# Kernel tuning notes

Measured on AMD Instinct MI355X. Metric: run time of the kernel, lower is better.

## Reference

```python
import jax, jax.numpy as jnp
import numpy as np
import math

D_MODEL = 1024
LAYER_ID = 6
NUM_LAYERS = 12
B, T = 8, 2048
MIN_P = -1e38


def _init_params():
    C = D_MODEL
    r01 = LAYER_ID / (NUM_LAYERS - 1)
    r1a0 = 1.0 - LAYER_ID / NUM_LAYERS
    h = np.arange(C, dtype=np.float32)
    decay_speed = -5.0 + 8.0 * (h / (C - 1)) ** (0.7 + 1.3 * r01)
    zigzag = (((np.arange(C) + 1) % 3) - 1).astype(np.float32) * 0.5
    U = np.float32(math.log(0.3)) + zigzag
    xx = (np.arange(C, dtype=np.float32) / C).reshape(1, 1, C)
    tmk = xx ** r1a0
    tmv = xx ** r1a0 + 0.3 * r01
    tmr = xx ** (0.5 * r1a0)
    return (jnp.asarray(decay_speed), jnp.asarray(U), jnp.asarray(tmk, jnp.float32),
            jnp.asarray(tmv, jnp.float32), jnp.asarray(tmr, jnp.float32))


def setup_inputs() -> dict:
    key = jax.random.key(0)
    k0, k1, k2, k3, k4 = jax.random.split(key, 5)
    W, U, tmk, tmv, tmr = _init_params()
    C = D_MODEL
    s = 1.0 / math.sqrt(C)
    return {
        "x": jax.random.normal(k0, (B, T, C), jnp.float32),
        "W": W, "U": U,
        "time_mix_k": tmk, "time_mix_v": tmv, "time_mix_r": tmr,
        "Wk": jax.random.normal(k1, (C, C), jnp.float32) * s,
        "Wv": jax.random.normal(k2, (C, C), jnp.float32) * s,
        "Wr": jax.random.normal(k3, (C, C), jnp.float32) * s,
        "Wo": jax.random.normal(k4, (C, C), jnp.float32) * s,
    }


def _wkv(W, U, k, v):
    # W, U: [C]; k, v: [B, T, C]. Stable WKV recurrence with max-trick.
    w = -jnp.exp(W)  # negative decay, per channel
    Bb, Tt, Cc = k.shape
    aa0 = jnp.zeros((Bb, Cc), k.dtype)
    bb0 = jnp.zeros((Bb, Cc), k.dtype)
    pp0 = jnp.full((Bb, Cc), MIN_P, k.dtype)

    def step(carry, kv_t):
        aa, bb, pp = carry
        kt, vt = kv_t  # [B, C]
        ww = U + kt
        p = jnp.maximum(pp, ww)
        e1 = jnp.exp(pp - p)
        e2 = jnp.exp(ww - p)
        y = (e1 * aa + e2 * vt) / (e1 * bb + e2)
        ww2 = pp + w
        p2 = jnp.maximum(ww2, kt)
        e1b = jnp.exp(ww2 - p2)
        e2b = jnp.exp(kt - p2)
        return (e1b * aa + e2b * vt, e1b * bb + e2b, p2), y

    kT = jnp.swapaxes(k, 0, 1)  # [T, B, C]
    vT = jnp.swapaxes(v, 0, 1)
    _, yT = jax.lax.scan(step, (aa0, bb0, pp0), (kT, vT))
    return jnp.swapaxes(yT, 0, 1)  # [B, T, C]


def reference(x, W, U, time_mix_k, time_mix_v, time_mix_r, Wk, Wv, Wr, Wo):
    # token shift: prepend zero along T, drop last step
    xs = jnp.pad(x, ((0, 0), (1, 0), (0, 0)))[:, :-1]
    xk = x * time_mix_k + xs * (1.0 - time_mix_k)
    xv = x * time_mix_v + xs * (1.0 - time_mix_v)
    xr = x * time_mix_r + xs * (1.0 - time_mix_r)
    K = jnp.einsum('btc,dc->btd', xk, Wk)
    V = jnp.einsum('btc,dc->btd', xv, Wv)
    R = jnp.einsum('btc,dc->btd', xr, Wr)
    wkv = _wkv(W, U, K, V)
    hidden = jax.lax.stop_gradient(wkv[:, -1, :])
    rwkv = jax.nn.sigmoid(R) * wkv
    output = jnp.einsum('btc,dc->btd', rwkv, Wo)
    return output, hidden
```

## Files before the change

### kernel.cpp

```cpp
#include <hip/hip_runtime.h>

#define Bn 8
#define Tn 2048
#define Cn 1024
#define Mn (Bn * Tn)
#define LCH 64
#define NCH (Tn / LCH)

typedef __attribute__((ext_vector_type(8))) short short8;
typedef __attribute__((ext_vector_type(4))) float f32x4;

typedef const __attribute__((address_space(1))) void gas_void;
typedef __attribute__((address_space(3))) void las_void;

__device__ __forceinline__ unsigned short f2bf(float f) {
    unsigned int u = __float_as_uint(f);
    u += 0x7FFFu + ((u >> 16) & 1u);
    return (unsigned short)(u >> 16);
}
__device__ __forceinline__ float bf2f(unsigned short h) {
    return __uint_as_float(((unsigned int)h) << 16);
}

__global__ __launch_bounds__(256) void cvt_kernel(const float* __restrict__ src,
                                                  unsigned short* __restrict__ dst) {
    int i = blockIdx.x * 256 + threadIdx.x;
    float4 v = ((const float4*)src)[i];
    ushort4 o;
    o.x = f2bf(v.x); o.y = f2bf(v.y); o.z = f2bf(v.z); o.w = f2bf(v.w);
    ((ushort4*)dst)[i] = o;
}

__device__ __forceinline__ ushort4 mix4(const float4& a, const float4& s, const float4& m) {
    ushort4 o;
    o.x = f2bf(s.x + (a.x - s.x) * m.x);
    o.y = f2bf(s.y + (a.y - s.y) * m.y);
    o.z = f2bf(s.z + (a.z - s.z) * m.z);
    o.w = f2bf(s.w + (a.w - s.w) * m.w);
    return o;
}

__global__ __launch_bounds__(256) void mix_kernel(const float* __restrict__ x,
                                                  const float* __restrict__ tmk,
                                                  const float* __restrict__ tmv,
                                                  const float* __restrict__ tmr,
                                                  unsigned short* __restrict__ ak,
                                                  unsigned short* __restrict__ av,
                                                  unsigned short* __restrict__ ar) {
    int i = blockIdx.x * 256 + threadIdx.x;
    int c4 = i & 255;
    int t  = (i >> 8) & (Tn - 1);
    float4 xc = ((const float4*)x)[i];
    float4 xs = make_float4(0.f, 0.f, 0.f, 0.f);
    if (t > 0) xs = ((const float4*)x)[i - 256];
    float4 mk = ((const float4*)tmk)[c4];
    float4 mv = ((const float4*)tmv)[c4];
    float4 mr = ((const float4*)tmr)[c4];
    ((ushort4*)ak)[i] = mix4(xc, xs, mk);
    ((ushort4*)av)[i] = mix4(xc, xs, mv);
    ((ushort4*)ar)[i] = mix4(xc, xs, mr);
}


#define BKg  32
#define NTg  32
#define ABYT (256 * BKg * 2)
#define BUFBY (2 * ABYT)

#define PHASE_BAR() asm volatile("s_barrier" ::: "memory")
#define WAITV4()    asm volatile("s_waitcnt vmcnt(4)" ::: "memory")
#define WAITV0()    asm volatile("s_waitcnt vmcnt(0)" ::: "memory")

__device__ __forceinline__ void stage16(const unsigned short* gbase,
                                        char* ldsdst, int lane) {
    int r = lane >> 2;
    int g = (lane & 3) ^ ((lane >> 3) & 3);
    const unsigned short* src = gbase + (size_t)r * 1024 + g * 8;
    __builtin_amdgcn_global_load_lds((gas_void*)src, (las_void*)ldsdst, 16, 0, 0);
}

__device__ __forceinline__ void gemm_body(int t,
    const unsigned short* __restrict__ A, const unsigned short* __restrict__ Bw,
    char* lds, int bm, int bn, int lane, int wid, int wr, int wc, int lr, int rsw,
    short8* afc, short8* bfc, short8* afn, short8* bfn, f32x4 acc[8][4]) {
    char* Ab = lds + (size_t)(t & 3) * BUFBY;
    char* Bb = Ab + ABYT;
    char* An = lds + (size_t)((t + 3) & 3) * BUFBY;
    char* Bs = An + ABYT;
    char* A1 = lds + (size_t)((t + 1) & 3) * BUFBY;
    char* B1 = A1 + ABYT;
    const bool st = (t + 3) < NTg;
    const bool ra = (t + 1) < NTg;
    const int k0 = (t + 3) * BKg;

    if (st) stage16(A + (size_t)(bm + wid * 16) * 1024 + k0, An + wid * 16 * 64, lane);
#pragma unroll
    for (int mi = 4; mi < 8; ++mi)
        afc[mi] = *(const short8*)(Ab + (wr * 128 + mi * 16 + lr) * 64 + rsw);
    __builtin_amdgcn_s_setprio(1);
#pragma unroll
    for (int mi = 0; mi < 2; ++mi)
#pragma unroll
        for (int ni = 0; ni < 4; ++ni)
            acc[mi][ni] = __builtin_amdgcn_mfma_f32_16x16x32_bf16(afc[mi], bfc[ni], acc[mi][ni], 0, 0, 0);
    __builtin_amdgcn_s_setprio(0);
    PHASE_BAR();

    if (st) stage16(A + (size_t)(bm + 128 + wid * 16) * 1024 + k0, An + (128 + wid * 16) * 64, lane);
    if (ra) {
#pragma unroll
        for (int ni = 0; ni < 4; ++ni)
            bfn[ni] = *(const short8*)(B1 + (wc * 64 + ni * 16 + lr) * 64 + rsw);
    }
    __builtin_amdgcn_s_setprio(1);
#pragma unroll
    for (int mi = 2; mi < 4; ++mi)
#pragma unroll
        for (int ni = 0; ni < 4; ++ni)
            acc[mi][ni] = __builtin_amdgcn_mfma_f32_16x16x32_bf16(afc[mi], bfc[ni], acc[mi][ni], 0, 0, 0);
    __builtin_amdgcn_s_setprio(0);
    PHASE_BAR();

    if (st) stage16(Bw + (size_t)(bn + wid * 16) * 1024 + k0, Bs + wid * 16 * 64, lane);
    if (ra) {
#pragma unroll
        for (int mi = 0; mi < 4; ++mi)
            afn[mi] = *(const short8*)(A1 + (wr * 128 + mi * 16 + lr) * 64 + rsw);
    }
    __builtin_amdgcn_s_setprio(1);
#pragma unroll
    for (int mi = 4; mi < 6; ++mi)
#pragma unroll
        for (int ni = 0; ni < 4; ++ni)
            acc[mi][ni] = __builtin_amdgcn_mfma_f32_16x16x32_bf16(afc[mi], bfc[ni], acc[mi][ni], 0, 0, 0);
    __builtin_amdgcn_s_setprio(0);
    PHASE_BAR();

    if (st) stage16(Bw + (size_t)(bn + 128 + wid * 16) * 1024 + k0, Bs + (128 + wid * 16) * 64, lane);
    __builtin_amdgcn_s_setprio(1);
#pragma unroll
    for (int mi = 6; mi < 8; ++mi)
#pragma unroll
        for (int ni = 0; ni < 4; ++ni)
            acc[mi][ni] = __builtin_amdgcn_mfma_f32_16x16x32_bf16(afc[mi], bfc[ni], acc[mi][ni], 0, 0, 0);
    __builtin_amdgcn_s_setprio(0);
    if (st) { WAITV4(); } else { WAITV0(); }
    PHASE_BAR();
}

template <int FOUT>
__global__ __launch_bounds__(512, 2) void gemm_bt(const unsigned short* __restrict__ A,
                                                  const unsigned short* __restrict__ Bw,
                                                  unsigned short* __restrict__ Cb,
                                                  float* __restrict__ Cf) {
    __shared__ char lds[4 * BUFBY];
    const int tid  = threadIdx.x;
    const int lane = tid & 63;
    const int wid  = tid >> 6;
    const int wr   = wid >> 2;
    const int wc   = wid & 3;
    const int bm   = blockIdx.x * 256;
    const int bn   = blockIdx.y * 256;

    const int lr  = lane & 15;
    const int rsw = (((lane >> 4) ^ ((lane >> 1) & 3)) << 4);

    f32x4 acc[8][4] = {};
    short8 afA[8], bfA[4], afB[8], bfB[4];

#pragma unroll
    for (int i = 0; i < 3; ++i) {
        char* Ad = lds + (size_t)i * BUFBY;
        int k0 = i * BKg;
        stage16(A  + (size_t)(bm + wid * 16) * 1024 + k0,       Ad + wid * 16 * 64, lane);
        stage16(A  + (size_t)(bm + 128 + wid * 16) * 1024 + k0, Ad + (128 + wid * 16) * 64, lane);
        stage16(Bw + (size_t)(bn + wid * 16) * 1024 + k0,       Ad + ABYT + wid * 16 * 64, lane);
        stage16(Bw + (size_t)(bn + 128 + wid * 16) * 1024 + k0, Ad + ABYT + (128 + wid * 16) * 64, lane);
    }
    WAITV4();
    PHASE_BAR();

#pragma unroll
    for (int mi = 0; mi < 4; ++mi)
        afA[mi] = *(const short8*)(lds + (wr * 128 + mi * 16 + lr) * 64 + rsw);
#pragma unroll
    for (int ni = 0; ni < 4; ++ni)
        bfA[ni] = *(const short8*)(lds + ABYT + (wc * 64 + ni * 16 + lr) * 64 + rsw);

#pragma unroll 1
    for (int t = 0; t < NTg; t += 2) {
        gemm_body(t,     A, Bw, lds, bm, bn, lane, wid, wr, wc, lr, rsw, afA, bfA, afB, bfB, acc);
        gemm_body(t + 1, A, Bw, lds, bm, bn, lane, wid, wr, wc, lr, rsw, afB, bfB, afA, bfA, acc);
    }

    const int crow0 = bm + wr * 128 + (lane >> 4) * 4;
    const int ccol0 = bn + wc * 64 + lr;
#pragma unroll
    for (int mi = 0; mi < 8; ++mi) {
#pragma unroll
        for (int ni = 0; ni < 4; ++ni) {
            int col = ccol0 + ni * 16;
#pragma unroll
            for (int j = 0; j < 4; ++j) {
                size_t idx = (size_t)(crow0 + mi * 16 + j) * 1024 + col;
                float v = acc[mi][ni][j];
                if (FOUT) Cf[idx] = v;
                else      Cb[idx] = f2bf(v);
            }
        }
    }
}

__global__ __launch_bounds__(256) void wkv_pass1(const unsigned short* __restrict__ K,
                                                 const unsigned short* __restrict__ V,
                                                 const float* __restrict__ Wd,
                                                 float* __restrict__ caa,
                                                 float* __restrict__ cbb,
                                                 float* __restrict__ cpp) {
    int c = blockIdx.x * 256 + threadIdx.x;
    int j = blockIdx.y;
    int b = blockIdx.z;
    float w = -__expf(Wd[c]);
    float aa = 0.f, bb = 0.f, pp = -1e38f;
    size_t base = ((size_t)(b * Tn + j * LCH)) * Cn + c;
#pragma unroll 4
    for (int t = 0; t < LCH; ++t) {
        size_t idx = base + (size_t)t * Cn;
        float kt = bf2f(K[idx]);
        float vt = bf2f(V[idx]);
        float ww2 = pp + w;
        float p2  = fmaxf(ww2, kt);
        float e1  = __expf(ww2 - p2);
        float e2  = __expf(kt - p2);
        aa = e1 * aa + e2 * vt;
        bb = e1 * bb + e2;
        pp = p2;
    }
    size_t o = ((size_t)b * NCH + j) * Cn + c;
    caa[o] = aa; cbb[o] = bb; cpp[o] = pp;
}

__global__ __launch_bounds__(256) void wkv_pass2(const float* __restrict__ Wd,
                                                 const float* __restrict__ caa,
                                                 const float* __restrict__ cbb,
                                                 const float* __restrict__ cpp,
                                                 float* __restrict__ saa,
                                                 float* __restrict__ sbb,
                                                 float* __restrict__ spp) {
    int c = blockIdx.x * 256 + threadIdx.x;
    int b = blockIdx.y;
    float Lw = -__expf(Wd[c]) * (float)LCH;
    float aa = 0.f, bb = 0.f, pp = -1e38f;
    for (int j = 0; j < NCH; ++j) {
        size_t o = ((size_t)b * NCH + j) * Cn + c;
        saa[o] = aa; sbb[o] = bb; spp[o] = pp;
        float qa = caa[o], qb = cbb[o], qp = cpp[o];
        float ppd = pp + Lw;
        float p  = fmaxf(ppd, qp);
        float e1 = __expf(ppd - p);
        float e2 = __expf(qp - p);
        aa = e1 * aa + e2 * qa;
        bb = e1 * bb + e2 * qb;
        pp = p;
    }
}

__global__ __launch_bounds__(256) void wkv_pass3(const unsigned short* __restrict__ K,
                                                 const unsigned short* __restrict__ V,
                                                 const unsigned short* __restrict__ Rb,
                                                 const float* __restrict__ Wd,
                                                 const float* __restrict__ Ud,
                                                 const float* __restrict__ saa,
                                                 const float* __restrict__ sbb,
                                                 const float* __restrict__ spp,
                                                 unsigned short* __restrict__ rwkv,
                                                 float* __restrict__ hidden) {
    int c = blockIdx.x * 256 + threadIdx.x;
    int j = blockIdx.y;
    int b = blockIdx.z;
    float w = -__expf(Wd[c]);
    float u = Ud[c];
    size_t o = ((size_t)b * NCH + j) * Cn + c;
    float aa = saa[o], bb = sbb[o], pp = spp[o];
    size_t base = ((size_t)(b * Tn + j * LCH)) * Cn + c;
    float y = 0.f;
#pragma unroll 4
    for (int t = 0; t < LCH; ++t) {
        size_t idx = base + (size_t)t * Cn;
        float kt = bf2f(K[idx]);
        float vt = bf2f(V[idx]);
        float rt = bf2f(Rb[idx]);
        float ww = u + kt;
        float p  = fmaxf(pp, ww);
        float e1 = __expf(pp - p);
        float e2 = __expf(ww - p);
        y = __fdividef(e1 * aa + e2 * vt, e1 * bb + e2);
        float sr = __fdividef(1.f, 1.f + __expf(-rt));
        rwkv[idx] = f2bf(sr * y);
        float ww2 = pp + w;
        float p2  = fmaxf(ww2, kt);
        float e1b = __expf(ww2 - p2);
        float e2b = __expf(kt - p2);
        aa = e1b * aa + e2b * vt;
        bb = e1b * bb + e2b;
        pp = p2;
    }
    if (j == NCH - 1) hidden[b * Cn + c] = y;
}

extern "C" void kernel_launch(void* const* d_in, const int* in_sizes, int n_in,
                              void* d_out, int out_size, void* d_ws, size_t ws_size,
                              hipStream_t stream) {
    const float* x   = (const float*)d_in[0];
    const float* Wd  = (const float*)d_in[1];
    const float* Ud  = (const float*)d_in[2];
    const float* tmk = (const float*)d_in[3];
    const float* tmv = (const float*)d_in[4];
    const float* tmr = (const float*)d_in[5];
    const float* Wk  = (const float*)d_in[6];
    const float* Wv  = (const float*)d_in[7];
    const float* Wr  = (const float*)d_in[8];
    const float* Wo  = (const float*)d_in[9];

    float* out    = (float*)d_out;
    float* hidden = out + (size_t)Mn * Cn;

    const size_t MK = (size_t)Mn * Cn;
    const size_t CC = (size_t)Cn * Cn;
    unsigned short* ak  = (unsigned short*)d_ws;
    unsigned short* av  = ak + MK;
    unsigned short* ar  = av + MK;
    unsigned short* Kb  = ar + MK;
    unsigned short* Wkb = Kb + MK;
    unsigned short* Wvb = Wkb + CC;
    unsigned short* Wrb = Wvb + CC;
    unsigned short* Wob = Wrb + CC;
    unsigned short* Vb = ak;
    unsigned short* Rb = av;
    unsigned short* rw = ar;
    const size_t SB = (size_t)Bn * NCH * Cn;
    float* caa = (float*)Wkb;
    float* cbb = caa + SB;
    float* cpp = cbb + SB;
    float* saa = cpp + SB;
    float* sbb = saa + SB;
    float* spp = sbb + SB;

    cvt_kernel<<<dim3(CC / 1024), 256, 0, stream>>>(Wk, Wkb);
    cvt_kernel<<<dim3(CC / 1024), 256, 0, stream>>>(Wv, Wvb);
    cvt_kernel<<<dim3(CC / 1024), 256, 0, stream>>>(Wr, Wrb);
    cvt_kernel<<<dim3(CC / 1024), 256, 0, stream>>>(Wo, Wob);

    mix_kernel<<<dim3(MK / 1024), 256, 0, stream>>>(x, tmk, tmv, tmr, ak, av, ar);

    dim3 gg(Mn / 256, Cn / 256);
    gemm_bt<0><<<gg, 512, 0, stream>>>(ak, Wkb, Kb, nullptr);
    gemm_bt<0><<<gg, 512, 0, stream>>>(av, Wvb, Vb, nullptr);
    gemm_bt<0><<<gg, 512, 0, stream>>>(ar, Wrb, Rb, nullptr);

    dim3 gw(Cn / 256, NCH, Bn);
    wkv_pass1<<<gw, 256, 0, stream>>>(Kb, Vb, Wd, caa, cbb, cpp);
    wkv_pass2<<<dim3(Cn / 256, Bn), 256, 0, stream>>>(Wd, caa, cbb, cpp, saa, sbb, spp);
    wkv_pass3<<<gw, 256, 0, stream>>>(Kb, Vb, Rb, Wd, Ud, saa, sbb, spp, rw, hidden);

    gemm_bt<1><<<gg, 512, 0, stream>>>(rw, Wob, nullptr, out);
}
```

Before: 362.3 us.

## Merge weight conversions, widen mix kernel, restructure GEMM main loop into two phases

The four weight-conversion launches are merged into a single launch using a 2D grid, and the token-mix kernel now handles 8 channels per thread with 16-byte bf16 stores. The GEMM inner body goes from four barrier-separated phases to two. Each phase issues two global-to-LDS stages and prefetches next-tile fragments before its MFMA block, and all 8 A fragments are preloaded up front. The aim is fewer barriers and launches and wider memory ops, at the cost of more live registers and less fine-grained interleaving of loads with MFMA.

Result: faster. 351.0 us (-3.1%).

```diff
diff --git a/kernel.cpp b/kernel.cpp
--- a/kernel.cpp
+++ b/kernel.cpp
@@ -8,6 +8,7 @@
 #define NCH (Tn / LCH)
 
 typedef __attribute__((ext_vector_type(8))) short short8;
+typedef __attribute__((ext_vector_type(8))) unsigned short u16x8;
 typedef __attribute__((ext_vector_type(4))) float f32x4;
 
 typedef const __attribute__((address_space(1))) void gas_void;
@@ -22,21 +23,36 @@
     return __uint_as_float(((unsigned int)h) << 16);
 }
 
-__global__ __launch_bounds__(256) void cvt_kernel(const float* __restrict__ src,
-                                                  unsigned short* __restrict__ dst) {
+__global__ __launch_bounds__(256) void cvt4_kernel(const float* __restrict__ s0,
+                                                   const float* __restrict__ s1,
+                                                   const float* __restrict__ s2,
+                                                   const float* __restrict__ s3,
+                                                   unsigned short* __restrict__ d0,
+                                                   unsigned short* __restrict__ d1,
+                                                   unsigned short* __restrict__ d2,
+                                                   unsigned short* __restrict__ d3) {
     int i = blockIdx.x * 256 + threadIdx.x;
+    int m = blockIdx.y;
+    const float* src = (m == 0) ? s0 : (m == 1) ? s1 : (m == 2) ? s2 : s3;
+    unsigned short* dst = (m == 0) ? d0 : (m == 1) ? d1 : (m == 2) ? d2 : d3;
     float4 v = ((const float4*)src)[i];
     ushort4 o;
     o.x = f2bf(v.x); o.y = f2bf(v.y); o.z = f2bf(v.z); o.w = f2bf(v.w);
     ((ushort4*)dst)[i] = o;
 }
 
-__device__ __forceinline__ ushort4 mix4(const float4& a, const float4& s, const float4& m) {
-    ushort4 o;
-    o.x = f2bf(s.x + (a.x - s.x) * m.x);
-    o.y = f2bf(s.y + (a.y - s.y) * m.y);
-    o.z = f2bf(s.z + (a.z - s.z) * m.z);
-    o.w = f2bf(s.w + (a.w - s.w) * m.w);
+__device__ __forceinline__ u16x8 mix8(const float4& a, const float4& b,
+                                      const float4& sa, const float4& sb,
+                                      const float4& ma, const float4& mb) {
+    u16x8 o;
+    o[0] = f2bf(sa.x + (a.x - sa.x) * ma.x);
+    o[1] = f2bf(sa.y + (a.y - sa.y) * ma.y);
+    o[2] = f2bf(sa.z + (a.z - sa.z) * ma.z);
+    o[3] = f2bf(sa.w + (a.w - sa.w) * ma.w);
+    o[4] = f2bf(sb.x + (b.x - sb.x) * mb.x);
+    o[5] = f2bf(sb.y + (b.y - sb.y) * mb.y);
+    o[6] = f2bf(sb.z + (b.z - sb.z) * mb.z);
+    o[7] = f2bf(sb.w + (b.w - sb.w) * mb.w);
     return o;
 }
 
@@ -48,17 +64,18 @@
                                                   unsigned short* __restrict__ av,
                                                   unsigned short* __restrict__ ar) {
     int i = blockIdx.x * 256 + threadIdx.x;
-    int c4 = i & 255;
-    int t  = (i >> 8) & (Tn - 1);
-    float4 xc = ((const float4*)x)[i];
-    float4 xs = make_float4(0.f, 0.f, 0.f, 0.f);
-    if (t > 0) xs = ((const float4*)x)[i - 256];
-    float4 mk = ((const float4*)tmk)[c4];
-    float4 mv = ((const float4*)tmv)[c4];
-    float4 mr = ((const float4*)tmr)[c4];
-    ((ushort4*)ak)[i] = mix4(xc, xs, mk);
-    ((ushort4*)av)[i] = mix4(xc, xs, mv);
-    ((ushort4*)ar)[i] = mix4(xc, xs, mr);
+    int c8 = i & 127;
+    int t  = (i >> 7) & (Tn - 1);
+    const float4* xp = (const float4*)x;
+    float4 xa = xp[2 * i], xb = xp[2 * i + 1];
+    float4 sa = make_float4(0.f, 0.f, 0.f, 0.f), sb = sa;
+    if (t > 0) { sa = xp[2 * i - 256]; sb = xp[2 * i - 255]; }
+    float4 ka = ((const float4*)tmk)[2 * c8], kb = ((const float4*)tmk)[2 * c8 + 1];
+    float4 va = ((const float4*)tmv)[2 * c8], vb = ((const float4*)tmv)[2 * c8 + 1];
+    float4 ra = ((const float4*)tmr)[2 * c8], rb = ((const float4*)tmr)[2 * c8 + 1];
+    ((u16x8*)ak)[i] = mix8(xa, xb, sa, sb, ka, kb);
+    ((u16x8*)av)[i] = mix8(xa, xb, sa, sb, va, vb);
+    ((u16x8*)ar)[i] = mix8(xa, xb, sa, sb, ra, rb);
 }
 
 
@@ -83,8 +100,6 @@
     const unsigned short* __restrict__ A, const unsigned short* __restrict__ Bw,
     char* lds, int bm, int bn, int lane, int wid, int wr, int wc, int lr, int rsw,
     short8* afc, short8* bfc, short8* afn, short8* bfn, f32x4 acc[8][4]) {
-    char* Ab = lds + (size_t)(t & 3) * BUFBY;
-    char* Bb = Ab + ABYT;
     char* An = lds + (size_t)((t + 3) & 3) * BUFBY;
     char* Bs = An + ABYT;
     char* A1 = lds + (size_t)((t + 1) & 3) * BUFBY;
@@ -93,53 +108,39 @@
     const bool ra = (t + 1) < NTg;
     const int k0 = (t + 3) * BKg;
 
-    if (st) stage16(A + (size_t)(bm + wid * 16) * 1024 + k0, An + wid * 16 * 64, lane);
-#pragma unroll
-    for (int mi = 4; mi < 8; ++mi)
-        afc[mi] = *(const short8*)(Ab + (wr * 128 + mi * 16 + lr) * 64 + rsw);
+    if (st) {
+        stage16(A + (size_t)(bm + wid * 16) * 1024 + k0,       An + wid * 16 * 64, lane);
+        stage16(A + (size_t)(bm + 128 + wid * 16) * 1024 + k0, An + (128 + wid * 16) * 64, lane);
+    }
+    if (ra) {
+#pragma unroll
+        for (int ni = 0; ni < 4; ++ni)
+            bfn[ni] = *(const short8*)(B1 + (wc * 64 + ni * 16 + lr) * 64 + rsw);
+#pragma unroll
+        for (int mi = 0; mi < 4; ++mi)
+            afn[mi] = *(const short8*)(A1 + (wr * 128 + mi * 16 + lr) * 64 + rsw);
+    }
     __builtin_amdgcn_s_setprio(1);
 #pragma unroll
-    for (int mi = 0; mi < 2; ++mi)
+    for (int mi = 0; mi < 4; ++mi)
 #pragma unroll
         for (int ni = 0; ni < 4; ++ni)
             acc[mi][ni] = __builtin_amdgcn_mfma_f32_16x16x32_bf16(afc[mi], bfc[ni], acc[mi][ni], 0, 0, 0);
     __builtin_amdgcn_s_setprio(0);
     PHASE_BAR();
 
-    if (st) stage16(A + (size_t)(bm + 128 + wid * 16) * 1024 + k0, An + (128 + wid * 16) * 64, lane);
+    if (st) {
+        stage16(Bw + (size_t)(bn + wid * 16) * 1024 + k0,       Bs + wid * 16 * 64, lane);
+        stage16(Bw + (size_t)(bn + 128 + wid * 16) * 1024 + k0, Bs + (128 + wid * 16) * 64, lane);
+    }
     if (ra) {
 #pragma unroll
-        for (int ni = 0; ni < 4; ++ni)
-            bfn[ni] = *(const short8*)(B1 + (wc * 64 + ni * 16 + lr) * 64 + rsw);
+        for (int mi = 4; mi < 8; ++mi)
+            afn[mi] = *(const short8*)(A1 + (wr * 128 + mi * 16 + lr) * 64 + rsw);
     }
     __builtin_amdgcn_s_setprio(1);
 #pragma unroll
-    for (int mi = 2; mi < 4; ++mi)
-#pragma unroll
-        for (int ni = 0; ni < 4; ++ni)
-            acc[mi][ni] = __builtin_amdgcn_mfma_f32_16x16x32_bf16(afc[mi], bfc[ni], acc[mi][ni], 0, 0, 0);
-    __builtin_amdgcn_s_setprio(0);
-    PHASE_BAR();
-
-    if (st) stage16(Bw + (size_t)(bn + wid * 16) * 1024 + k0, Bs + wid * 16 * 64, lane);
-    if (ra) {
-#pragma unroll
-        for (int mi = 0; mi < 4; ++mi)
-            afn[mi] = *(const short8*)(A1 + (wr * 128 + mi * 16 + lr) * 64 + rsw);
-    }
-    __builtin_amdgcn_s_setprio(1);
-#pragma unroll
-    for (int mi = 4; mi < 6; ++mi)
-#pragma unroll
-        for (int ni = 0; ni < 4; ++ni)
-            acc[mi][ni] = __builtin_amdgcn_mfma_f32_16x16x32_bf16(afc[mi], bfc[ni], acc[mi][ni], 0, 0, 0);
-    __builtin_amdgcn_s_setprio(0);
-    PHASE_BAR();
-
-    if (st) stage16(Bw + (size_t)(bn + 128 + wid * 16) * 1024 + k0, Bs + (128 + wid * 16) * 64, lane);
-    __builtin_amdgcn_s_setprio(1);
-#pragma unroll
-    for (int mi = 6; mi < 8; ++mi)
+    for (int mi = 4; mi < 8; ++mi)
 #pragma unroll
         for (int ni = 0; ni < 4; ++ni)
             acc[mi][ni] = __builtin_amdgcn_mfma_f32_16x16x32_bf16(afc[mi], bfc[ni], acc[mi][ni], 0, 0, 0);
@@ -181,7 +182,7 @@
     PHASE_BAR();
 
 #pragma unroll
-    for (int mi = 0; mi < 4; ++mi)
+    for (int mi = 0; mi < 8; ++mi)
         afA[mi] = *(const short8*)(lds + (wr * 128 + mi * 16 + lr) * 64 + rsw);
 #pragma unroll
     for (int ni = 0; ni < 4; ++ni)
@@ -346,12 +347,9 @@
     float* sbb = saa + SB;
     float* spp = sbb + SB;
 
-    cvt_kernel<<<dim3(CC / 1024), 256, 0, stream>>>(Wk, Wkb);
-    cvt_kernel<<<dim3(CC / 1024), 256, 0, stream>>>(Wv, Wvb);
-    cvt_kernel<<<dim3(CC / 1024), 256, 0, stream>>>(Wr, Wrb);
-    cvt_kernel<<<dim3(CC / 1024), 256, 0, stream>>>(Wo, Wob);
-
-    mix_kernel<<<dim3(MK / 1024), 256, 0, stream>>>(x, tmk, tmv, tmr, ak, av, ar);
+    cvt4_kernel<<<dim3(CC / 1024, 4), 256, 0, stream>>>(Wk, Wv, Wr, Wo, Wkb, Wvb, Wrb, Wob);
+
+    mix_kernel<<<dim3(MK / 2048), 256, 0, stream>>>(x, tmk, tmv, tmr, ak, av, ar);
 
     dim3 gg(Mn / 256, Cn / 256);
     gemm_bt<0><<<gg, 512, 0, stream>>>(ak, Wkb, Kb, nullptr);
```
